# Kernel optimization log

Hardware: AMD Instinct MI355X
Metric: run time of the kernel (lower is better)

The kernel has to match this reference:

```python
import jax, jax.numpy as jnp
import numpy as np

N_WIRES = 8
DIM = 1 << N_WIRES  # 256
ENC_WIRES = [0, 1, 2, 2, 4, 5, 6, 7]  # faithful to source: wire 2 twice, wire 3 skipped

# Precompute composed CNOT-ring permutation: CNOT(0,1),(1,2),...,(6,7),(7,0)
_idx = np.arange(DIM)
_perm = _idx.copy()
for c, t in [(k, k + 1) for k in range(N_WIRES - 1)] + [(N_WIRES - 1, 0)]:
    cbit = (_idx >> (N_WIRES - 1 - c)) & 1
    P = np.where(cbit == 1, _idx ^ (1 << (N_WIRES - 1 - t)), _idx)
    _perm = _perm[P]
CNOT_PERM = jnp.asarray(_perm)
# Pauli-Z sign table per wire: (8, 256)
Z_SIGNS = jnp.asarray(1 - 2 * ((_idx[None, :] >> (N_WIRES - 1 - np.arange(N_WIRES)[:, None])) & 1)).astype(jnp.float32)


def _rx(state, wire, theta):
    """Apply RX(theta) on `wire`. state: (N, 256) complex64, theta: (N,) float."""
    N = state.shape[0]
    s = state.reshape(N, 1 << wire, 2, 1 << (N_WIRES - 1 - wire))
    half = theta * 0.5
    c = jnp.cos(half)[:, None, None]
    sn = jnp.sin(half)[:, None, None]
    a, b = s[:, :, 0, :], s[:, :, 1, :]
    top = c * a - 1j * sn * b
    bot = -1j * sn * a + c * b
    return jnp.stack([top, bot], axis=2).reshape(N, DIM)


def qlayer(tokens, theta):
    """Batched 8-qubit circuit: encoder RX(x_k), trainable RX(theta_w), CNOT ring, <Z_w>.
    tokens: (N, 8) float32 -> (N, 8) float32 expectation values."""
    N = tokens.shape[0]
    state = jnp.zeros((N, DIM), jnp.complex64).at[:, 0].set(1.0)
    for k, w in enumerate(ENC_WIRES):
        state = _rx(state, w, tokens[:, k])
    for w in range(N_WIRES):
        state = _rx(state, w, jnp.broadcast_to(theta[w], (N,)))
    state = state[:, CNOT_PERM]
    probs = state.real ** 2 + state.imag ** 2  # (N, 256)
    return probs @ Z_SIGNS.T  # (N, 8)


def setup_inputs() -> dict:
    key = jax.random.key(0)
    kx, kt = jax.random.split(key)
    x = jax.random.normal(kx, (16, 1024, 8), dtype=jnp.float32)
    theta = jax.random.uniform(kt, (8,), dtype=jnp.float32, minval=0.0, maxval=2.0 * np.pi)
    return {"x": x, "theta": theta}


def reference(x, theta):
    B, S, E = x.shape
    H, dk = 2, E // 2
    tok = x.reshape(B * S, E)
    # Original computes Q, K, V with the SAME shared q_layer on the SAME input,
    # so Q == K == V; compute once.
    qkv = qlayer(tok, theta).reshape(B, S, E)
    h = qkv.reshape(B, S, H, dk).transpose(0, 2, 1, 3)  # (B,H,S,dk)
    scores = jnp.einsum('bhqd,bhkd->bhqk', h, h) / np.sqrt(dk).astype(np.float32)
    w = jax.nn.softmax(scores, axis=-1)  # (eval mode: dropout inactive)
    attn = jnp.einsum('bhqk,bhkd->bhqd', w, h)
    concat = attn.transpose(0, 2, 1, 3).reshape(B, S, E)
    out = qlayer(concat.reshape(B * S, E), theta).reshape(B, S, E)
    return out
```

## Files before the change

### kernel.cpp

```cpp
#include <hip/hip_runtime.h>

#define SEQ 1024

typedef __attribute__((ext_vector_type(2))) float f2;

static __device__ __forceinline__ int slot_addr(int s) {
    return (s ^ ((s >> 6) & 7)) << 2;
}

static __device__ __forceinline__ void qrow(const float th[8], const float y[8], float o[8]) {
    float a[8];
    a[0] = y[0] + th[0];
    a[1] = y[1] + th[1];
    a[2] = y[2] + y[3] + th[2];
    a[3] = th[3];
    a[4] = y[4] + th[4];
    a[5] = y[5] + th[5];
    a[6] = y[6] + th[6];
    a[7] = y[7] + th[7];
    float c[8];
#pragma unroll
    for (int w = 0; w < 8; ++w) c[w] = __cosf(a[w]);
    o[1] = c[0] * c[1];
#pragma unroll
    for (int w = 2; w < 8; ++w) o[w] = o[w - 1] * c[w];
    float s = c[7];
#pragma unroll
    for (int w = 6; w >= 1; --w) s *= c[w];
    o[0] = s;
}

__global__ __launch_bounds__(256, 2) void mhaq_fused(const float* __restrict__ x,
                                                     const float* __restrict__ theta,
                                                     float* __restrict__ out) {
    __shared__ __align__(16) float smem[11264 + 320];
    float* const res = smem + 11264;

    const int b   = blockIdx.x >> 5;
    const int qof = (blockIdx.x & 31) << 5;
    const int t   = threadIdx.x;

    float th[8];
#pragma unroll
    for (int w = 0; w < 8; ++w) th[w] = theta[w];

    const float4* xb = (const float4*)(x + (size_t)b * SEQ * 8);
    float4 v0[4], v1[4];
#pragma unroll
    for (int r = 0; r < 4; ++r) {
        const int k = t + (r << 8);
        v0[r] = xb[2 * k];
        v1[r] = xb[2 * k + 1];
    }
#pragma unroll
    for (int r = 0; r < 4; ++r) {
        const int k = t + (r << 8);
        const float y[8] = {v0[r].x, v0[r].y, v0[r].z, v0[r].w,
                            v1[r].x, v1[r].y, v1[r].z, v1[r].w};
        float o[8];
        qrow(th, y, o);
        *(float4*)&smem[slot_addr(2 * k)]     = make_float4(o[0], o[1], o[2], o[3]);
        *(float4*)&smem[slot_addr(2 * k + 1)] = make_float4(o[4], o[5], o[6], o[7]);
    }
    __syncthreads();

    const int lane = t & 63;
    const int wv   = t >> 6;
    const int qs   = wv >> 1;
    const int kh   = wv & 1;
    const int g    = lane >> 4;
    const int m    = lane & 15;
    const int q0   = qof + (qs << 4) + (g << 2);

    const float qscale = 0.5f * 1.44269504f;
    f2 qv[4][4];
#pragma unroll
    for (int qq = 0; qq < 4; ++qq) {
        const float4 qa = *(const float4*)&smem[slot_addr(2 * (q0 + qq))];
        const float4 qb = *(const float4*)&smem[slot_addr(2 * (q0 + qq) + 1)];
        qv[qq][0] = f2{qa.x, qa.y} * qscale;
        qv[qq][1] = f2{qa.z, qa.w} * qscale;
        qv[qq][2] = f2{qb.x, qb.y} * qscale;
        qv[qq][3] = f2{qb.z, qb.w} * qscale;
    }

    float l0[4] = {0.f, 0.f, 0.f, 0.f};
    float l1[4] = {0.f, 0.f, 0.f, 0.f};
    f2 a01[4], a23[4], a45[4], a67[4];
#pragma unroll
    for (int qq = 0; qq < 4; ++qq) {
        a01[qq] = f2{0.f, 0.f};
        a23[qq] = f2{0.f, 0.f};
        a45[qq] = f2{0.f, 0.f};
        a67[qq] = f2{0.f, 0.f};
    }

    const int kbase = (kh << 9) + (m << 5);
#pragma unroll 4
    for (int i = 0; i < 32; ++i) {
        const int s0 = (kbase + i) << 1;
        const float4 k0 = *(const float4*)&smem[slot_addr(s0)];
        const float4 k1 = *(const float4*)&smem[slot_addr(s0 + 1)];
        const f2 k01 = {k0.x, k0.y}, k23 = {k0.z, k0.w};
        const f2 k45 = {k1.x, k1.y}, k67 = {k1.z, k1.w};
#pragma unroll
        for (int qq = 0; qq < 4; ++qq) {
            const f2 d0 = qv[qq][0] * k01 + qv[qq][1] * k23;
            const f2 d1 = qv[qq][2] * k45 + qv[qq][3] * k67;
            const float e0 = __builtin_amdgcn_exp2f(d0.x + d0.y);
            const float e1 = __builtin_amdgcn_exp2f(d1.x + d1.y);
            l0[qq] += e0;
            l1[qq] += e1;
            const f2 e0v = {e0, e0}, e1v = {e1, e1};
            a01[qq] += e0v * k01;
            a23[qq] += e0v * k23;
            a45[qq] += e1v * k45;
            a67[qq] += e1v * k67;
        }
    }
    __syncthreads();

    {
        float buf[40];
#pragma unroll
        for (int qq = 0; qq < 4; ++qq) {
            buf[qq * 10 + 0] = l0[qq];
            buf[qq * 10 + 1] = l1[qq];
            buf[qq * 10 + 2] = a01[qq].x;
            buf[qq * 10 + 3] = a01[qq].y;
            buf[qq * 10 + 4] = a23[qq].x;
            buf[qq * 10 + 5] = a23[qq].y;
            buf[qq * 10 + 6] = a45[qq].x;
            buf[qq * 10 + 7] = a45[qq].y;
            buf[qq * 10 + 8] = a67[qq].x;
            buf[qq * 10 + 9] = a67[qq].y;
        }
        float4* pp = (float4*)&smem[t * 44];
#pragma unroll
        for (int i = 0; i < 10; ++i) pp[i] = ((const float4*)buf)[i];
    }
    __syncthreads();

    for (int u = t; u < 320; u += 256) {
        const int q  = u / 10;
        const int j  = u - q * 10;
        const int uqs = q >> 4, ug = (q >> 2) & 3, uqq = q & 3;
        const int base = ((uqs << 7) + (ug << 4)) * 44 + uqq * 10 + j;
        float s = 0.f;
#pragma unroll
        for (int mm = 0; mm < 16; ++mm)
            s += smem[base + mm * 44] + smem[base + (64 + mm) * 44];
        res[q * 10 + j] = s;
    }
    __syncthreads();

    if (t < 32) {
        const float* r = &res[t * 10];
        const float inv0 = 1.0f / r[0];
        const float inv1 = 1.0f / r[1];
        const float y[8] = {r[2] * inv0, r[3] * inv0, r[4] * inv0, r[5] * inv0,
                            r[6] * inv1, r[7] * inv1, r[8] * inv1, r[9] * inv1};
        float o[8];
        qrow(th, y, o);
        float4* op = (float4*)(out + ((size_t)(b * SEQ + qof + t)) * 8);
        op[0] = make_float4(o[0], o[1], o[2], o[3]);
        op[1] = make_float4(o[4], o[5], o[6], o[7]);
    }
}

extern "C" void kernel_launch(void* const* d_in, const int* in_sizes, int n_in,
                              void* d_out, int out_size, void* d_ws, size_t ws_size,
                              hipStream_t stream) {
    const float* x     = (const float*)d_in[0];
    const float* theta = (const float*)d_in[1];
    float* out         = (float*)d_out;
    mhaq_fused<<<dim3(512), dim3(256), 0, stream>>>(x, theta, out);
}
```

Baseline: 65.72 us.

## Double threads per block and reduce partial sums with wave shuffles

Raises the block size from 256 to 512 threads so each thread handles 2 query rows instead of 4, and each thread covers a different slice of the keys. The partial softmax sums are first combined across 4 neighbouring lanes with xor shuffles, then written to a small shared buffer that 32 threads sum. This drops one barrier and the large per-thread shared-memory dump. The aim is more parallelism per block and less reduction traffic, at the cost of recomputing the token transform in more threads and a larger block under a register budget of 4 blocks per CU.

After: 66.41 us. No clear change (+1.0%).

```diff
diff --git a/kernel.cpp b/kernel.cpp
--- a/kernel.cpp
+++ b/kernel.cpp
@@ -30,11 +30,11 @@
     o[0] = s;
 }
 
-__global__ __launch_bounds__(256, 2) void mhaq_fused(const float* __restrict__ x,
+__global__ __launch_bounds__(512, 4) void mhaq_fused(const float* __restrict__ x,
                                                      const float* __restrict__ theta,
                                                      float* __restrict__ out) {
-    __shared__ __align__(16) float smem[11264 + 320];
-    float* const res = smem + 11264;
+    __shared__ __align__(16) float smem[8192 + 2560];
+    float* const part = smem + 8192;
 
     const int b   = blockIdx.x >> 5;
     const int qof = (blockIdx.x & 31) << 5;
@@ -45,18 +45,18 @@
     for (int w = 0; w < 8; ++w) th[w] = theta[w];
 
     const float4* xb = (const float4*)(x + (size_t)b * SEQ * 8);
-    float4 v0[4], v1[4];
+    float4 va[2], vb[2];
 #pragma unroll
-    for (int r = 0; r < 4; ++r) {
-        const int k = t + (r << 8);
-        v0[r] = xb[2 * k];
-        v1[r] = xb[2 * k + 1];
+    for (int r = 0; r < 2; ++r) {
+        const int k = t + (r << 9);
+        va[r] = xb[2 * k];
+        vb[r] = xb[2 * k + 1];
     }
 #pragma unroll
-    for (int r = 0; r < 4; ++r) {
-        const int k = t + (r << 8);
-        const float y[8] = {v0[r].x, v0[r].y, v0[r].z, v0[r].w,
-                            v1[r].x, v1[r].y, v1[r].z, v1[r].w};
+    for (int r = 0; r < 2; ++r) {
+        const int k = t + (r << 9);
+        const float y[8] = {va[r].x, va[r].y, va[r].z, va[r].w,
+                            vb[r].x, vb[r].y, vb[r].z, vb[r].w};
         float o[8];
         qrow(th, y, o);
         *(float4*)&smem[slot_addr(2 * k)]     = make_float4(o[0], o[1], o[2], o[3]);
@@ -70,12 +70,12 @@
     const int kh   = wv & 1;
     const int g    = lane >> 4;
     const int m    = lane & 15;
-    const int q0   = qof + (qs << 4) + (g << 2);
+    const int q0   = qof + (qs << 3) + (g << 1);
 
     const float qscale = 0.5f * 1.44269504f;
-    f2 qv[4][4];
+    f2 qv[2][4];
 #pragma unroll
-    for (int qq = 0; qq < 4; ++qq) {
+    for (int qq = 0; qq < 2; ++qq) {
         const float4 qa = *(const float4*)&smem[slot_addr(2 * (q0 + qq))];
         const float4 qb = *(const float4*)&smem[slot_addr(2 * (q0 + qq) + 1)];
         qv[qq][0] = f2{qa.x, qa.y} * qscale;
@@ -84,27 +84,27 @@
         qv[qq][3] = f2{qb.z, qb.w} * qscale;
     }
 
-    float l0[4] = {0.f, 0.f, 0.f, 0.f};
-    float l1[4] = {0.f, 0.f, 0.f, 0.f};
-    f2 a01[4], a23[4], a45[4], a67[4];
+    float l0[2] = {0.f, 0.f};
+    float l1[2] = {0.f, 0.f};
+    f2 a01[2], a23[2], a45[2], a67[2];
 #pragma unroll
-    for (int qq = 0; qq < 4; ++qq) {
+    for (int qq = 0; qq < 2; ++qq) {
         a01[qq] = f2{0.f, 0.f};
         a23[qq] = f2{0.f, 0.f};
         a45[qq] = f2{0.f, 0.f};
         a67[qq] = f2{0.f, 0.f};
     }
 
-    const int kbase = (kh << 9) + (m << 5);
+    const int sbase = (kh << 10) + (m << 6);
 #pragma unroll 4
     for (int i = 0; i < 32; ++i) {
-        const int s0 = (kbase + i) << 1;
+        const int s0 = sbase + (i << 1);
         const float4 k0 = *(const float4*)&smem[slot_addr(s0)];
         const float4 k1 = *(const float4*)&smem[slot_addr(s0 + 1)];
         const f2 k01 = {k0.x, k0.y}, k23 = {k0.z, k0.w};
         const f2 k45 = {k1.x, k1.y}, k67 = {k1.z, k1.w};
 #pragma unroll
-        for (int qq = 0; qq < 4; ++qq) {
+        for (int qq = 0; qq < 2; ++qq) {
             const f2 d0 = qv[qq][0] * k01 + qv[qq][1] * k23;
             const f2 d1 = qv[qq][2] * k45 + qv[qq][3] * k67;
             const float e0 = __builtin_amdgcn_exp2f(d0.x + d0.y);
@@ -118,44 +118,50 @@
             a67[qq] += e1v * k67;
         }
     }
-    __syncthreads();
 
-    {
-        float buf[40];
+    float buf[20];
 #pragma unroll
-        for (int qq = 0; qq < 4; ++qq) {
-            buf[qq * 10 + 0] = l0[qq];
-            buf[qq * 10 + 1] = l1[qq];
-            buf[qq * 10 + 2] = a01[qq].x;
-            buf[qq * 10 + 3] = a01[qq].y;
-            buf[qq * 10 + 4] = a23[qq].x;
-            buf[qq * 10 + 5] = a23[qq].y;
-            buf[qq * 10 + 6] = a45[qq].x;
-            buf[qq * 10 + 7] = a45[qq].y;
-            buf[qq * 10 + 8] = a67[qq].x;
-            buf[qq * 10 + 9] = a67[qq].y;
-        }
-        float4* pp = (float4*)&smem[t * 44];
+    for (int qq = 0; qq < 2; ++qq) {
+        buf[qq * 10 + 0] = l0[qq];
+        buf[qq * 10 + 1] = l1[qq];
+        buf[qq * 10 + 2] = a01[qq].x;
+        buf[qq * 10 + 3] = a01[qq].y;
+        buf[qq * 10 + 4] = a23[qq].x;
+        buf[qq * 10 + 5] = a23[qq].y;
+        buf[qq * 10 + 6] = a45[qq].x;
+        buf[qq * 10 + 7] = a45[qq].y;
+        buf[qq * 10 + 8] = a67[qq].x;
+        buf[qq * 10 + 9] = a67[qq].y;
+    }
 #pragma unroll
-        for (int i = 0; i < 10; ++i) pp[i] = ((const float4*)buf)[i];
+    for (int j = 0; j < 20; ++j) {
+        float v = buf[j];
+        v += __shfl_xor(v, 1, 64);
+        v += __shfl_xor(v, 2, 64);
+        buf[j] = v;
     }
-    __syncthreads();
 
-    for (int u = t; u < 320; u += 256) {
-        const int q  = u / 10;
-        const int j  = u - q * 10;
-        const int uqs = q >> 4, ug = (q >> 2) & 3, uqq = q & 3;
-        const int base = ((uqs << 7) + (ug << 4)) * 44 + uqq * 10 + j;
-        float s = 0.f;
+    if ((m & 3) == 0) {
+        const int rid = (wv << 4) + (g << 2) + (m >> 2);
+        float4* pp = (float4*)&part[rid * 20];
 #pragma unroll
-        for (int mm = 0; mm < 16; ++mm)
-            s += smem[base + mm * 44] + smem[base + (64 + mm) * 44];
-        res[q * 10 + j] = s;
+        for (int ii = 0; ii < 5; ++ii) pp[ii] = ((const float4*)buf)[ii];
     }
     __syncthreads();
 
     if (t < 32) {
-        const float* r = &res[t * 10];
+        const int qs2 = t >> 3, g2 = (t >> 1) & 3, qq = t & 1;
+        float r[10];
+#pragma unroll
+        for (int j = 0; j < 10; ++j) {
+            float s = 0.f;
+#pragma unroll
+            for (int kh2 = 0; kh2 < 2; ++kh2)
+#pragma unroll
+                for (int mv = 0; mv < 4; ++mv)
+                    s += part[((((qs2 << 1) + kh2) << 4) + (g2 << 2) + mv) * 20 + qq * 10 + j];
+            r[j] = s;
+        }
         const float inv0 = 1.0f / r[0];
         const float inv1 = 1.0f / r[1];
         const float y[8] = {r[2] * inv0, r[3] * inv0, r[4] * inv0, r[5] * inv0,
@@ -174,5 +180,5 @@
     const float* x     = (const float*)d_in[0];
     const float* theta = (const float*)d_in[1];
     float* out         = (float*)d_out;
-    mhaq_fused<<<dim3(512), dim3(256), 0, stream>>>(x, theta, out);
+    mhaq_fused<<<dim3(512), dim3(512), 0, stream>>>(x, theta, out);
 }
```

## Repack Q pairs for packed math, shuffle-reduce partials, shrink LDS for occupancy

Applied to the files above, without the earlier changes.

Moves the partial-sum staging into a separate smaller LDS region so the shared array shrinks, and raises the launch-bounds occupancy hint to 4 blocks per CU. The inner loop now packs two queries per f2 lane for packed FMA and exp, fully unrolls the key loop, and computes K addresses with an XOR instead of recomputing slot_addr. Partial results are reduced across groups of 4 lanes with shuffles before a single lane writes them, which removes one barrier and shortens the final reduction. The higher occupancy target may force register spills given the many accumulators.

Result: no change. 65.49 us (-0.3%).

```diff
diff --git a/kernel.cpp b/kernel.cpp
--- a/kernel.cpp
+++ b/kernel.cpp
@@ -30,11 +30,12 @@
     o[0] = s;
 }
 
-__global__ __launch_bounds__(256, 2) void mhaq_fused(const float* __restrict__ x,
+__global__ __launch_bounds__(256, 4) void mhaq_fused(const float* __restrict__ x,
                                                      const float* __restrict__ theta,
                                                      float* __restrict__ out) {
-    __shared__ __align__(16) float smem[11264 + 320];
-    float* const res = smem + 11264;
+    __shared__ __align__(16) float smem[8192 + 2816 + 320];
+    float* const part = smem + 8192;
+    float* const res  = part + 2816;
 
     const int b   = blockIdx.x >> 5;
     const int qof = (blockIdx.x & 31) << 5;
@@ -73,20 +74,29 @@
     const int q0   = qof + (qs << 4) + (g << 2);
 
     const float qscale = 0.5f * 1.44269504f;
-    f2 qv[4][4];
+    float4 qa[4], qb[4];
 #pragma unroll
     for (int qq = 0; qq < 4; ++qq) {
-        const float4 qa = *(const float4*)&smem[slot_addr(2 * (q0 + qq))];
-        const float4 qb = *(const float4*)&smem[slot_addr(2 * (q0 + qq) + 1)];
-        qv[qq][0] = f2{qa.x, qa.y} * qscale;
-        qv[qq][1] = f2{qa.z, qa.w} * qscale;
-        qv[qq][2] = f2{qb.x, qb.y} * qscale;
-        qv[qq][3] = f2{qb.z, qb.w} * qscale;
-    }
-
-    float l0[4] = {0.f, 0.f, 0.f, 0.f};
-    float l1[4] = {0.f, 0.f, 0.f, 0.f};
+        qa[qq] = *(const float4*)&smem[slot_addr(2 * (q0 + qq))];
+        qb[qq] = *(const float4*)&smem[slot_addr(2 * (q0 + qq) + 1)];
+    }
+    f2 pk0[2][4], pk1[2][4];
+#pragma unroll
+    for (int p = 0; p < 2; ++p) {
+        pk0[p][0] = f2{qa[2 * p].x, qa[2 * p + 1].x} * qscale;
+        pk0[p][1] = f2{qa[2 * p].y, qa[2 * p + 1].y} * qscale;
+        pk0[p][2] = f2{qa[2 * p].z, qa[2 * p + 1].z} * qscale;
+        pk0[p][3] = f2{qa[2 * p].w, qa[2 * p + 1].w} * qscale;
+        pk1[p][0] = f2{qb[2 * p].x, qb[2 * p + 1].x} * qscale;
+        pk1[p][1] = f2{qb[2 * p].y, qb[2 * p + 1].y} * qscale;
+        pk1[p][2] = f2{qb[2 * p].z, qb[2 * p + 1].z} * qscale;
+        pk1[p][3] = f2{qb[2 * p].w, qb[2 * p + 1].w} * qscale;
+    }
+
+    f2 lp0[2], lp1[2];
     f2 a01[4], a23[4], a45[4], a67[4];
+#pragma unroll
+    for (int p = 0; p < 2; ++p) { lp0[p] = f2{0.f, 0.f}; lp1[p] = f2{0.f, 0.f}; }
 #pragma unroll
     for (int qq = 0; qq < 4; ++qq) {
         a01[qq] = f2{0.f, 0.f};
@@ -95,62 +105,84 @@
         a67[qq] = f2{0.f, 0.f};
     }
 
-    const int kbase = (kh << 9) + (m << 5);
-#pragma unroll 4
+    const int sbase = (kh << 10) + (m << 6);
+    const int abase = slot_addr(sbase);
+#pragma unroll
     for (int i = 0; i < 32; ++i) {
-        const int s0 = (kbase + i) << 1;
-        const float4 k0 = *(const float4*)&smem[slot_addr(s0)];
-        const float4 k1 = *(const float4*)&smem[slot_addr(s0 + 1)];
+        const float4 k0 = *(const float4*)&smem[abase ^ (i << 3)];
+        const float4 k1 = *(const float4*)&smem[abase ^ ((i << 3) | 4)];
         const f2 k01 = {k0.x, k0.y}, k23 = {k0.z, k0.w};
         const f2 k45 = {k1.x, k1.y}, k67 = {k1.z, k1.w};
 #pragma unroll
-        for (int qq = 0; qq < 4; ++qq) {
-            const f2 d0 = qv[qq][0] * k01 + qv[qq][1] * k23;
-            const f2 d1 = qv[qq][2] * k45 + qv[qq][3] * k67;
-            const float e0 = __builtin_amdgcn_exp2f(d0.x + d0.y);
-            const float e1 = __builtin_amdgcn_exp2f(d1.x + d1.y);
-            l0[qq] += e0;
-            l1[qq] += e1;
-            const f2 e0v = {e0, e0}, e1v = {e1, e1};
-            a01[qq] += e0v * k01;
-            a23[qq] += e0v * k23;
-            a45[qq] += e1v * k45;
-            a67[qq] += e1v * k67;
+        for (int p = 0; p < 2; ++p) {
+            f2 d0 = pk0[p][0] * f2{k0.x, k0.x};
+            d0 += pk0[p][1] * f2{k0.y, k0.y};
+            d0 += pk0[p][2] * f2{k0.z, k0.z};
+            d0 += pk0[p][3] * f2{k0.w, k0.w};
+            f2 d1 = pk1[p][0] * f2{k1.x, k1.x};
+            d1 += pk1[p][1] * f2{k1.y, k1.y};
+            d1 += pk1[p][2] * f2{k1.z, k1.z};
+            d1 += pk1[p][3] * f2{k1.w, k1.w};
+            f2 e0, e1;
+            e0.x = __builtin_amdgcn_exp2f(d0.x);
+            e0.y = __builtin_amdgcn_exp2f(d0.y);
+            e1.x = __builtin_amdgcn_exp2f(d1.x);
+            e1.y = __builtin_amdgcn_exp2f(d1.y);
+            lp0[p] += e0;
+            lp1[p] += e1;
+            a01[2 * p]     += f2{e0.x, e0.x} * k01;
+            a23[2 * p]     += f2{e0.x, e0.x} * k23;
+            a01[2 * p + 1] += f2{e0.y, e0.y} * k01;
+            a23[2 * p + 1] += f2{e0.y, e0.y} * k23;
+            a45[2 * p]     += f2{e1.x, e1.x} * k45;
+            a67[2 * p]     += f2{e1.x, e1.x} * k67;
+            a45[2 * p + 1] += f2{e1.y, e1.y} * k45;
+            a67[2 * p + 1] += f2{e1.y, e1.y} * k67;
         }
     }
-    __syncthreads();
-
-    {
-        float buf[40];
-#pragma unroll
-        for (int qq = 0; qq < 4; ++qq) {
-            buf[qq * 10 + 0] = l0[qq];
-            buf[qq * 10 + 1] = l1[qq];
-            buf[qq * 10 + 2] = a01[qq].x;
-            buf[qq * 10 + 3] = a01[qq].y;
-            buf[qq * 10 + 4] = a23[qq].x;
-            buf[qq * 10 + 5] = a23[qq].y;
-            buf[qq * 10 + 6] = a45[qq].x;
-            buf[qq * 10 + 7] = a45[qq].y;
-            buf[qq * 10 + 8] = a67[qq].x;
-            buf[qq * 10 + 9] = a67[qq].y;
-        }
-        float4* pp = (float4*)&smem[t * 44];
-#pragma unroll
-        for (int i = 0; i < 10; ++i) pp[i] = ((const float4*)buf)[i];
+
+    float buf[40];
+#pragma unroll
+    for (int qq = 0; qq < 4; ++qq) {
+        const int p = qq >> 1, hi = qq & 1;
+        buf[qq * 10 + 0] = hi ? lp0[p].y : lp0[p].x;
+        buf[qq * 10 + 1] = hi ? lp1[p].y : lp1[p].x;
+        buf[qq * 10 + 2] = a01[qq].x;
+        buf[qq * 10 + 3] = a01[qq].y;
+        buf[qq * 10 + 4] = a23[qq].x;
+        buf[qq * 10 + 5] = a23[qq].y;
+        buf[qq * 10 + 6] = a45[qq].x;
+        buf[qq * 10 + 7] = a45[qq].y;
+        buf[qq * 10 + 8] = a67[qq].x;
+        buf[qq * 10 + 9] = a67[qq].y;
+    }
+#pragma unroll
+    for (int j = 0; j < 40; ++j) {
+        float v = buf[j];
+        v += __shfl_xor(v, 1, 64);
+        v += __shfl_xor(v, 2, 64);
+        buf[j] = v;
+    }
+
+    if ((m & 3) == 0) {
+        const int rid = (wv << 4) + (g << 2) + (m >> 2);
+        float4* pp = (float4*)&part[rid * 44];
+#pragma unroll
+        for (int ii = 0; ii < 10; ++ii) pp[ii] = ((const float4*)buf)[ii];
     }
     __syncthreads();
 
     for (int u = t; u < 320; u += 256) {
         const int q  = u / 10;
         const int j  = u - q * 10;
-        const int uqs = q >> 4, ug = (q >> 2) & 3, uqq = q & 3;
-        const int base = ((uqs << 7) + (ug << 4)) * 44 + uqq * 10 + j;
+        const int qs2 = q >> 4, g2 = (q >> 2) & 3, qq = q & 3;
         float s = 0.f;
 #pragma unroll
-        for (int mm = 0; mm < 16; ++mm)
-            s += smem[base + mm * 44] + smem[base + (64 + mm) * 44];
-        res[q * 10 + j] = s;
+        for (int kh2 = 0; kh2 < 2; ++kh2)
+#pragma unroll
+            for (int mm = 0; mm < 4; ++mm)
+                s += part[((((qs2 << 1) + kh2) << 4) + (g2 << 2) + mm) * 44 + qq * 10 + j];
+        res[u] = s;
     }
     __syncthreads();
 
```
